# Performance work log

Measured on AMD Instinct MI355X. Metric: run time of the kernel, lower is better.

The kernel has to match this reference:

```python
import jax, jax.numpy as jnp
import numpy as np

LAG_SEQ = [1, 2, 3, 4, 5, 6, 7, 14, 21, 28]
MAX_LAG = 28
N_LAGS = 10
HID = 64
B, L, C = 256, 412, 3
CTX, HOR, NS = 336, 48, 100
IN_DIM = 15  # target + 10 lags + emb + last feat + log-scale + (C-2) mid feats


def lstm_cell(x, h, c, W_ih, W_hh, b_ih, b_hh):
    g = x @ W_ih.T + b_ih + h @ W_hh.T + b_hh
    i, f, gg, o = jnp.split(g, 4, axis=-1)
    c = jax.nn.sigmoid(f) * c + jax.nn.sigmoid(i) * jnp.tanh(gg)
    h = jax.nn.sigmoid(o) * jnp.tanh(c)
    return h, c


def lstm_layer(x, h, c, W_ih, W_hh, b_ih, b_hh):
    # x: [B, T, I] -> out [B, T, HID]; PyTorch gate order i,f,g,o
    xp = x @ W_ih.T + b_ih
    def step(carry, xt):
        h, c = carry
        g = xt + h @ W_hh.T + b_hh
        i, f, gg, o = jnp.split(g, 4, axis=-1)
        c = jax.nn.sigmoid(f) * c + jax.nn.sigmoid(i) * jnp.tanh(gg)
        h = jax.nn.sigmoid(o) * jnp.tanh(c)
        return (h, c), h
    (h, c), ys = jax.lax.scan(step, (h, c), jnp.swapaxes(xp, 0, 1))
    return jnp.swapaxes(ys, 0, 1), h, c


def head(out, w_df, b_df, w_loc, b_loc, w_scale, b_scale):
    # GluonTS-style StudentT output head
    df = 2.0 + jax.nn.softplus(jnp.dot(out, w_df) + b_df)
    loc = jnp.dot(out, w_loc) + b_loc
    scale = jax.nn.softplus(jnp.dot(out, w_scale) + b_scale)
    return df, loc, scale


def student_t_noise(key, df):
    kz, kg = jax.random.split(key)
    z = jax.random.normal(kz, df.shape, dtype=df.dtype)
    g = jax.random.gamma(kg, df * 0.5)  # chi2(df) = 2 * gamma(df/2)
    return z * jnp.sqrt(df / (2.0 * g))


def deepar_forward(X, pad_mask, W_ih0, W_hh0, b_ih0, b_hh0, W_ih1, W_hh1, b_ih1, b_hh1,
                   w_df, b_df, w_loc, b_loc, w_scale, b_scale, emb, H, context_length, n_samples):
    lag_idx = jnp.array(LAG_SEQ)
    Bd, Ld, Cd = X.shape
    ctx = context_length
    # zero out future targets, reversed observed target
    X = X.at[:, -H:, 0].set(0.0)
    past_target = jnp.flip(X[:, :-H, 0], axis=1)              # [B, L-H], newest first
    X = X[:, MAX_LAG:, :]
    pad_mask = pad_mask[:, MAX_LAG:]
    T = Ld - MAX_LAG
    # masked mean-abs scaling over the context window
    m = pad_mask[:, :ctx, None].astype(X.dtype)
    tscale = jnp.sum(jnp.abs(X[:, :ctx, :1]) * m, axis=1, keepdims=True) / jnp.maximum(
        jnp.sum(m, axis=1, keepdims=True), 1.0)
    tscale = jnp.maximum(tscale, 1e-10)                       # [B,1,1]
    Xs = X.at[:, :, 0].set(X[:, :, 0] / tscale[:, :, 0])
    past_target = past_target / tscale[:, :, 0]
    # context lags: step t gathers past_target[:, lag_seq + t], then flip over t
    idx = lag_idx[None, :] + jnp.arange(ctx)[:, None]         # [ctx, N_LAGS]
    ctx_lags = jnp.flip(past_target[:, idx], axis=1)          # [B, ctx, N_LAGS]
    lags = jnp.zeros((Bd, T, N_LAGS), X.dtype).at[:, :ctx].set(ctx_lags)
    emb_feat = jnp.broadcast_to(emb[0, 0], (Bd, T, 1))
    log_scale = jnp.broadcast_to(jnp.log(tscale[:, :, :1]), (Bd, T, 1))
    Xc = jnp.concatenate([Xs[:, :, :1], lags, emb_feat, Xs[:, :, -1:], log_scale,
                          Xs[:, :, 1:-1]], axis=2)            # [B, T, IN_DIM]
    inp = Xc[:, :-1, :]
    # context encoding with 2-layer LSTM
    z = jnp.zeros((Bd, HID), X.dtype)
    out0, h0, c0 = lstm_layer(inp[:, :ctx], z, z, W_ih0, W_hh0, b_ih0, b_hh0)
    out1, h1, c1 = lstm_layer(out0, z, z, W_ih1, W_hh1, b_ih1, b_hh1)
    df, loc, sc = head(out1, w_df, b_df, w_loc, b_loc, w_scale, b_scale)  # [B, ctx]
    # repeat_interleave over samples
    rep = lambda a: jnp.repeat(a, n_samples, axis=0)
    df, loc, sc = rep(df), rep(loc), rep(sc)
    tscale_flat = rep(tscale[:, 0, 0])                        # [NSB]
    key = jax.random.key(42)
    k_ctx, k_loop = jax.random.split(key)
    y_ctx = (loc + sc * student_t_noise(k_ctx, df)) * tscale_flat[:, None]  # [NSB, ctx]
    rows = jnp.swapaxes(rep(inp[:, ctx:ctx + H - 1, :]), 0, 1)  # [H-1, NSB, IN_DIM]
    buf0 = rep(past_target[:, :MAX_LAG])                       # [NSB, MAX_LAG]
    h0r, c0r, h1r, c1r = rep(h0), rep(c0), rep(h1), rep(c1)
    keys = jax.random.split(k_loop, H - 1)

    def step(carry, xt):
        prev, buf, h0, c0, h1, c1 = carry
        row, k = xt
        new_scaled = prev / tscale_flat
        buf2 = jnp.concatenate([new_scaled[:, None], buf], axis=1)  # [NSB, MAX_LAG+1]
        lag_f = buf2[:, lag_idx]                                    # [NSB, N_LAGS]
        row = row.at[:, 0].set(new_scaled)
        row = jax.lax.dynamic_update_slice(row, lag_f, (0, 1))
        row = jax.lax.stop_gradient(row)  # mirrors .clone().detach() in torch loop
        h0n, c0n = lstm_cell(row, h0, c0, W_ih0, W_hh0, b_ih0, b_hh0)
        h1n, c1n = lstm_cell(h0n, h1, c1, W_ih1, W_hh1, b_ih1, b_hh1)
        d, l, s = head(h1n, w_df, b_df, w_loc, b_loc, w_scale, b_scale)  # [NSB]
        y = (l + s * student_t_noise(k, d)) * tscale_flat
        return (y, buf2[:, :MAX_LAG], h0n, c0n, h1n, c1n), y

    init = (y_ctx[:, -1], buf0, h0r, c0r, h1r, c1r)
    _, ys = jax.lax.scan(step, init, (rows, keys))
    y_hat = jnp.concatenate([y_ctx, jnp.swapaxes(ys, 0, 1)], axis=1)  # [NSB, T-1]
    y_hat = y_hat.reshape(Bd, n_samples, T - 1)
    # torch.median returns the lower middle element for even n
    med = jnp.sort(y_hat, axis=1)[:, (n_samples - 1) // 2, :]
    return med[:, :, None]                                    # [B, T-1, 1]


def setup_inputs():
    key = jax.random.key(0)
    ks = jax.random.split(key, 20)
    rn = lambda k, shape, s=0.08: jax.random.normal(k, shape, dtype=jnp.float32) * s
    return {
        "X": jax.random.normal(ks[0], (B, L, C), dtype=jnp.float32),
        "pad_mask": jnp.ones((B, L), dtype=bool),
        "W_ih0": rn(ks[1], (4 * HID, IN_DIM)), "W_hh0": rn(ks[2], (4 * HID, HID)),
        "b_ih0": rn(ks[3], (4 * HID,)), "b_hh0": rn(ks[4], (4 * HID,)),
        "W_ih1": rn(ks[5], (4 * HID, HID)), "W_hh1": rn(ks[6], (4 * HID, HID)),
        "b_ih1": rn(ks[7], (4 * HID,)), "b_hh1": rn(ks[8], (4 * HID,)),
        "w_df": rn(ks[9], (HID,)), "b_df": rn(ks[10], ()),
        "w_loc": rn(ks[11], (HID,)), "b_loc": rn(ks[12], ()),
        "w_scale": rn(ks[13], (HID,)), "b_scale": rn(ks[14], ()),
        "emb": rn(ks[15], (1, 1)),
        "H": HOR, "context_length": CTX, "n_samples": NS,
    }


def reference(X, pad_mask, W_ih0, W_hh0, b_ih0, b_hh0, W_ih1, W_hh1, b_ih1, b_hh1,
              w_df, b_df, w_loc, b_loc, w_scale, b_scale, emb, H, context_length, n_samples):
    return deepar_forward(X, pad_mask, W_ih0, W_hh0, b_ih0, b_hh0, W_ih1, W_hh1, b_ih1, b_hh1,
                          w_df, b_df, w_loc, b_loc, w_scale, b_scale, emb,
                          H, context_length, n_samples)
```

## Files before the change

kernel.cpp:

```cpp
#include <hip/hip_runtime.h>
#include <stdint.h>
#include <stddef.h>

typedef uint32_t u32;
typedef float v2f __attribute__((ext_vector_type(2)));
typedef _Float16 f16;
typedef f16 half8 __attribute__((ext_vector_type(8)));
typedef float floatx4 __attribute__((ext_vector_type(4)));

#define NB    256
#define LFULL 412
#define NCH   3
#define CTX   336
#define NSAMP 100
#define TM1   383
#define HID   64
#define NIN   15
#define RTOT  25600
#define NCTXS 8601600u
#define NSTEP 47

#define DROWS   128
#define RPW     16
#define DBLOCKS (RTOT / DROWS)

#define HSTR    72

#define JAX_PARTITIONABLE 1

__device__ const int c_LAGS[10] = {1,2,3,4,5,6,7,14,21,28};

__device__ inline v2f bc2(float x) { v2f r; r[0] = x; r[1] = x; return r; }

__host__ __device__ inline void tf2x32(u32 k0, u32 k1, u32 x0, u32 x1, u32& o0, u32& o1) {
  const u32 ks2 = k0 ^ k1 ^ 0x1BD11BDAu;
#define TFR(r) { x0 += x1; x1 = (x1 << (r)) | (x1 >> (32 - (r))); x1 ^= x0; }
  x0 += k0; x1 += k1;
  TFR(13) TFR(15) TFR(26) TFR(6)
  x0 += k1; x1 += ks2 + 1u;
  TFR(17) TFR(29) TFR(16) TFR(24)
  x0 += ks2; x1 += k0 + 2u;
  TFR(13) TFR(15) TFR(26) TFR(6)
  x0 += k0; x1 += k1 + 3u;
  TFR(17) TFR(29) TFR(16) TFR(24)
  x0 += k1; x1 += ks2 + 4u;
  TFR(13) TFR(15) TFR(26) TFR(6)
  x0 += ks2; x1 += k0 + 5u;
#undef TFR
  o0 = x0; o1 = x1;
}

__host__ __device__ inline u32 split_word_legacy(u32 k0, u32 k1, u32 n, u32 j) {
  u32 o0, o1;
  if (j < n) { tf2x32(k0, k1, j, n + j, o0, o1); return o0; }
  tf2x32(k0, k1, j - n, j, o0, o1); return o1;
}

__host__ __device__ inline void jx_subkey(u32 k0, u32 k1, u32 n, u32 i, u32& s0, u32& s1) {
#if JAX_PARTITIONABLE
  (void)n; tf2x32(k0, k1, 0u, i, s0, s1);
#else
  s0 = split_word_legacy(k0, k1, n, 2u * i);
  s1 = split_word_legacy(k0, k1, n, 2u * i + 1u);
#endif
}
// ... 72 lines not shown
    u32 nk0, nk1, xk0, xk1, uk0, uk1;
    jx_subkey(K0, K1, 3u, 0u, nk0, nk1);
    jx_subkey(K0, K1, 3u, 1u, xk0, xk1);
    jx_subkey(K0, K1, 3u, 2u, uk0, uk1);
    K0 = nk0; K1 = nk1;
    float x, v;
    u32 c0 = xk0, c1 = xk1;
    do {
      u32 t0, t1, s0, s1;
      jx_subkey(c0, c1, 2u, 0u, t0, t1);
      jx_subkey(c0, c1, 2u, 1u, s0, s1);
      c0 = t0; c1 = t1;
      x = normal_from_bits(jx_bits(s0, s1, 1u, 0u));
      v = 1.0f + x * c;
    } while (v <= 0.0f);
    X = x * x;
    V = (v * v) * v;
    U = u01_from_bits(jx_bits(uk0, uk1, 1u, 0u));
  }
  const float sample = d * V;
  const float boost = boost_mask ? 1.0f : powf(u_boost, 1.0f / alpha_orig);
  return sample * boost;
}

__device__ inline float sigm(float x) {
  return __builtin_amdgcn_rcpf(1.0f + exp2f(-1.44269504f * x));
}
__device__ inline float tanh_fast(float x) {
  const float e = exp2f(2.88539008f * x);
  return 1.0f - 2.0f * __builtin_amdgcn_rcpf(e + 1.0f);
}
__device__ inline float softplusf(float x) { return fmaxf(x, 0.0f) + log1pf(expf(-fabsf(x))); }

__device__ inline float rl_f(float v, int l) {
  return __int_as_float(__builtin_amdgcn_readlane(__float_as_int(v), l));
}

enum : size_t {
  OFF_INP  = 0,
  OFF_CT   = OFF_INP + (size_t)NB * TM1 * NIN,
  OFF_TS   = OFF_CT + (size_t)NB * CTX,
  OFF_LTS  = OFF_TS + NB,
  OFF_DF   = OFF_LTS + NB,
  OFF_LOC  = OFF_DF + (size_t)NB * CTX,
  OFF_SC   = OFF_LOC + (size_t)NB * CTX,
  OFF_H0F  = OFF_SC + (size_t)NB * CTX,
  OFF_C0F  = OFF_H0F + (size_t)NB * HID,
  OFF_H1F  = OFF_C0F + (size_t)NB * HID,
  OFF_C1F  = OFF_H1F + (size_t)NB * HID,
  OFF_YH   = OFF_C1F + (size_t)NB * HID,
  OFF_WTX  = OFF_YH + (size_t)RTOT * TM1,
  OFF_WT00 = OFF_WTX + 4096,
  OFF_WT10 = OFF_WT00 + 16384,
  OFF_WT11 = OFF_WT10 + 16384,
  OFF_WH   = OFF_WT11 + 16384,
  OFF_RND  = OFF_WH + 27136,
  WS_FLOATS = OFF_RND + (size_t)NSTEP * RTOT * 4
};

#define WH_X   0
#define WH_00  4096
#define WH_10  20480
#define WH_11  36864
#define WH_HD  53248
#define WH_TOT 54272

__global__ void __launch_bounds__(256) wtrans_kernel(
    const float* __restrict__ Wih0, const float* __restrict__ Whh0,
    const float* __restrict__ Wih1, const float* __restrict__ Whh1,
    float* __restrict__ WTx, float* __restrict__ WT00,
    float* __restrict__ WT10, float* __restrict__ WT11)
{
  const int i = blockIdx.x * 256 + threadIdx.x;
  if (i < 4096) {
    const int k = i >> 8, g = i & 255;
    WTx[i] = (k < 15) ? Wih0[g * 15 + k] : 0.0f;
  } else if (i < 4096 + 16384) {
    const int j = i - 4096, k = j >> 8, g = j & 255;
    WT00[j] = Whh0[g * 64 + k];
  } else if (i < 4096 + 32768) {
    const int j = i - 4096 - 16384, k = j >> 8, g = j & 255;
    WT10[j] = Wih1[g * 64 + k];
  } else {
    const int j = i - 4096 - 32768, k = j >> 8, g = j & 255;
    WT11[j] = Whh1[g * 64 + k];
  }
}

__global__ void __launch_bounds__(256) wh_kernel(
    const float* __restrict__ Wih0, const float* __restrict__ Whh0,
    const float* __restrict__ Wih1, const float* __restrict__ Whh1,
    const float* __restrict__ bih0, const float* __restrict__ bhh0,
    const float* __restrict__ wdf, const float* __restrict__ wloc,
    const float* __restrict__ wsc,
    f16* __restrict__ WH)
{
  const int j = blockIdx.x * 256 + threadIdx.x;
  if (j < WH_00) {
    const int nt = j >> 8, rem = j & 255;
    const int l = rem >> 3, e = rem & 7;
    const int g = nt * 16 + (l & 15);
    const int k = (l >> 4) * 8 + e;
    WH[j] = (f16)((k < 15) ? Wih0[g * 15 + k] : (bih0[g] + bhh0[g]));
  } else if (j < WH_HD) {
    const float* W; int q;
    if (j < WH_10)      { W = Whh0; q = j - WH_00; }
    else if (j < WH_11) { W = Wih1; q = j - WH_10; }
    else                { W = Whh1; q = j - WH_11; }
    const int blk = q >> 9, rem = q & 511;
    const int l = rem >> 3, e = rem & 7;
    const int nt = blk >> 1, kc = blk & 1;
    const int g = nt * 16 + (l & 15);
    const int k = kc * 32 + (l >> 4) * 8 + e;
    WH[j] = (f16)W[g * 64 + k];
  } else {
    const int q = j - WH_HD;
    const int kc = q >> 9, rem = q & 511;
    const int l = rem >> 3, e = rem & 7;
    const int n = l & 15;
    const int k = kc * 32 + (l >> 4) * 8 + e;
// ... 10 lines not shown
{
  const int i = blockIdx.x * 256 + threadIdx.x;
  const int s = i / RTOT, rg = i - s * RTOT;
  u32 ks0, ks1, skz0, skz1, skg0, skg1;
  tf2x32(kl0, kl1, 0u, (u32)s, ks0, ks1);
  tf2x32(ks0, ks1, 0u, 0u, skz0, skz1);
  tf2x32(ks0, ks1, 0u, 1u, skg0, skg1);
  const float z = normal_from_bits(jx_bits(skz0, skz1, RTOT, (u32)rg));
  u32 gk0, gk1;
  jx_subkey(skg0, skg1, RTOT, (u32)rg, gk0, gk1);
  u32 K0, K1, S0, S1;
  jx_subkey(gk0, gk1, 2u, 0u, K0, K1);
  jx_subkey(gk0, gk1, 2u, 1u, S0, S1);
  u32 nk0, nk1, xk0, xk1, uk0, uk1;
  jx_subkey(K0, K1, 3u, 0u, nk0, nk1);
  jx_subkey(K0, K1, 3u, 1u, xk0, xk1);
  jx_subkey(K0, K1, 3u, 2u, uk0, uk1);
  u32 c0 = xk0, c1 = xk1, t0, t1, s0, s1;
  jx_subkey(c0, c1, 2u, 0u, t0, t1);
  jx_subkey(c0, c1, 2u, 1u, s0, s1);
  const float x1 = normal_from_bits(jx_bits(s0, s1, 1u, 0u));
  c0 = t0; c1 = t1;
  jx_subkey(c0, c1, 2u, 0u, t0, t1);
  jx_subkey(c0, c1, 2u, 1u, s0, s1);
  const float x2 = normal_from_bits(jx_bits(s0, s1, 1u, 0u));
  const float U1 = u01_from_bits(jx_bits(uk0, uk1, 1u, 0u));
  float* R = RND + (size_t)i * 4;
  R[0] = z; R[1] = x1; R[2] = x2; R[3] = U1;
}

__global__ void __launch_bounds__(256) prep_kernel(
    const float* __restrict__ X, const float* __restrict__ emb,
    float* __restrict__ inp, float* __restrict__ ct,
    float* __restrict__ tscale, float* __restrict__ ltscale)
{
  const int b = blockIdx.x, t = threadIdx.x;
  __shared__ float red[256];
  __shared__ float ts_sh;
  const float* Xb = X + (size_t)b * LFULL * NCH;
  float p = fabsf(Xb[(28 + t) * NCH]);
  if (t < 80) p += fabsf(Xb[(28 + 256 + t) * NCH]);
  red[t] = p;
  for (int st = 128; st > 0; st >>= 1) { __syncthreads(); if (t < st) red[t] += red[t + st]; }
  __syncthreads();
  if (t == 0) {
    float ts = red[0] / 336.0f;
    ts = fmaxf(ts, 1e-10f);
    tscale[b] = ts; ltscale[b] = logf(ts); ts_sh = ts;
  }
  __syncthreads();
  const float ts = ts_sh;
  const float lts = logf(ts);
  const float ev = emb[0];
  for (int idx = t; idx < TM1 * NIN; idx += 256) {
    const int tt = idx / NIN, f = idx - tt * NIN;
    float val;
    if (f == 0)       val = (tt < CTX) ? Xb[(28 + tt) * NCH] / ts : 0.0f;
    else if (f <= 10) val = (tt < CTX) ? Xb[(28 + tt - c_LAGS[f - 1]) * NCH] / ts : 0.0f;
    else if (f == 11) val = ev;
    else if (f == 12) val = Xb[(28 + tt) * NCH + 2];
    else if (f == 13) val = lts;
    else              val = Xb[(28 + tt) * NCH + 1];
    inp[(size_t)(b * TM1 + tt) * NIN + f] = val;
    if (f == 0 && tt < CTX) ct[b * CTX + tt] = val;
  }
}

__global__ void __launch_bounds__(256) ctx_lstm_kernel(
    const float* __restrict__ inp,
    const float* __restrict__ WTx, const float* __restrict__ WT00,
    const float* __restrict__ WT10, const float* __restrict__ WT11,
    const float* __restrict__ bih0, const float* __restrict__ bhh0,
    const float* __restrict__ bih1, const float* __restrict__ bhh1,
    const float* __restrict__ wdf, const float* __restrict__ bdfp,
    const float* __restrict__ wloc, const float* __restrict__ blocp,
    const float* __restrict__ wsc, const float* __restrict__ bscp,
    float* __restrict__ dfo, float* __restrict__ loco, float* __restrict__ sco,
    float* __restrict__ h0f, float* __restrict__ c0f,
    float* __restrict__ h1f, float* __restrict__ c1f)
{
  const int b = blockIdx.x, t = threadIdx.x;
  const int lane = t & 63, w = t >> 6;
  const int gbase = lane << 2;
  __shared__ __align__(16) float gA[4][256];
  __shared__ __align__(16) float gB[4][256];

  const float bs0 = bih0[lane]       + bhh0[lane];
  const float bs1 = bih0[64 + lane]  + bhh0[64 + lane];
  const float bs2 = bih0[128 + lane] + bhh0[128 + lane];
  const float bs3 = bih0[192 + lane] + bhh0[192 + lane];
  const float bs4 = bih1[lane]       + bhh1[lane];
  const float bs5 = bih1[64 + lane]  + bhh1[64 + lane];
  const float bs6 = bih1[128 + lane] + bhh1[128 + lane];
  const float bs7 = bih1[192 + lane] + bhh1[192 + lane];
  const float wdfv = wdf[lane], wlocv = wloc[lane], wscv = wsc[lane];
  const float bdf = bdfp[0], bloc = blocp[0], bsc = bscp[0];

  float h0r = 0.f, h1r = 0.f, c0r = 0.f, c1r = 0.f;
  const float* inb = inp + (size_t)b * TM1 * NIN;
  const int kx = w * 4;
  const int kh = w * 16;

  for (int tt = 0; tt < CTX; tt++) {
    float xr = 0.f;
    if (lane < 15) xr = inb[tt * NIN + lane];

    v2f aA = bc2(0.0f), aB = bc2(0.0f);
#pragma unroll
    for (int kk = 0; kk < 4; kk++) {
      const int k = kx + kk;
      const float4 wv = *(const float4*)&WTx[(k << 8) + gbase];
      v2f wlo, whi; wlo[0] = wv.x; wlo[1] = wv.y; whi[0] = wv.z; whi[1] = wv.w;
      const v2f hk = bc2(rl_f(xr, k));
      aA += wlo * hk; aB += whi * hk;
    }
#pragma unroll
    for (int kk = 0; kk < 16; kk++) {
      const int k = kh + kk;
      const float4 wv = *(const float4*)&WT00[(k << 8) + gbase];
      v2f wlo, whi; wlo[0] = wv.x; wlo[1] = wv.y; whi[0] = wv.z; whi[1] = wv.w;
      const v2f hk = bc2(rl_f(h0r, k));
      aA += wlo * hk; aB += whi * hk;
    }
    {
      float4 gv; gv.x = aA[0]; gv.y = aA[1]; gv.z = aB[0]; gv.w = aB[1];
      *(float4*)&gA[w][gbase] = gv;
    }
    __syncthreads();

    {
      float gi = ((gA[0][lane]       + gA[1][lane])       + gA[2][lane])       + gA[3][lane];
      float gf = ((gA[0][64 + lane]  + gA[1][64 + lane])  + gA[2][64 + lane])  + gA[3][64 + lane];
      float gg = ((gA[0][128 + lane] + gA[1][128 + lane]) + gA[2][128 + lane]) + gA[3][128 + lane];
      float go = ((gA[0][192 + lane] + gA[1][192 + lane]) + gA[2][192 + lane]) + gA[3][192 + lane];
      gi += bs0; gf += bs1; gg += bs2; go += bs3;
      c0r = sigm(gf) * c0r + sigm(gi) * tanh_fast(gg);
      h0r = sigm(go) * tanh_fast(c0r);
    }

    aA = bc2(0.0f); aB = bc2(0.0f);
#pragma unroll
    for (int kk = 0; kk < 16; kk++) {
      const int k = kh + kk;
      const float4 wv = *(const float4*)&WT10[(k << 8) + gbase];
      v2f wlo, whi; wlo[0] = wv.x; wlo[1] = wv.y; whi[0] = wv.z; whi[1] = wv.w;
      const v2f hk = bc2(rl_f(h0r, k));
      aA += wlo * hk; aB += whi * hk;
    }
#pragma unroll
    for (int kk = 0; kk < 16; kk++) {
      const int k = kh + kk;
      const float4 wv = *(const float4*)&WT11[(k << 8) + gbase];
      v2f wlo, whi; wlo[0] = wv.x; wlo[1] = wv.y; whi[0] = wv.z; whi[1] = wv.w;
      const v2f hk = bc2(rl_f(h1r, k));
      aA += wlo * hk; aB += whi * hk;
    }
    {
      float4 gv; gv.x = aA[0]; gv.y = aA[1]; gv.z = aB[0]; gv.w = aB[1];
      *(float4*)&gB[w][gbase] = gv;
    }
    __syncthreads();

    {
      float gi = ((gB[0][lane]       + gB[1][lane])       + gB[2][lane])       + gB[3][lane];
      float gf = ((gB[0][64 + lane]  + gB[1][64 + lane])  + gB[2][64 + lane])  + gB[3][64 + lane];
      float gg = ((gB[0][128 + lane] + gB[1][128 + lane]) + gB[2][128 + lane]) + gB[3][128 + lane];
      float go = ((gB[0][192 + lane] + gB[1][192 + lane]) + gB[2][192 + lane]) + gB[3][192 + lane];
      gi += bs4; gf += bs5; gg += bs6; go += bs7;
      c1r = sigm(gf) * c1r + sigm(gi) * tanh_fast(gg);
      h1r = sigm(go) * tanh_fast(c1r);
      if (w == 0) {
        float pd = h1r * wdfv, pl = h1r * wlocv, ps = h1r * wscv;
#pragma unroll
        for (int off = 32; off > 0; off >>= 1) {
          pd += __shfl_down(pd, off, 64);
          pl += __shfl_down(pl, off, 64);
          ps += __shfl_down(ps, off, 64);
        }
        if (lane == 0) {
          dfo[b * CTX + tt]  = 2.0f + softplusf(pd + bdf);
          loco[b * CTX + tt] = pl + bloc;
          sco[b * CTX + tt]  = softplusf(ps + bsc);
        }
      }
    }
  }
  if (w == 0) {
    h0f[b * 64 + lane] = h0r; c0f[b * 64 + lane] = c0r;
    h1f[b * 64 + lane] = h1r; c1f[b * 64 + lane] = c1r;
  }
}

__global__ void __launch_bounds__(256) ctx_sample_kernel(
    const float* __restrict__ df, const float* __restrict__ loc, const float* __restrict__ sc,
    const float* __restrict__ tscale, float* __restrict__ yhat,
    u32 kz0, u32 kz1, u32 kg0, u32 kg1)
{
  const int i = blockIdx.x * 256 + threadIdx.x;
  const int r = i / CTX, t = i - r * CTX;
  const int b = r / NSAMP;
  const float dfv = df[b * CTX + t], lv = loc[b * CTX + t], sv = sc[b * CTX + t];
  const float z = normal_from_bits(jx_bits(kz0, kz1, NCTXS, (u32)i));
  u32 gk0, gk1;
  jx_subkey(kg0, kg1, NCTXS, (u32)i, gk0, gk1);
  const float g = jax_gamma_one(gk0, gk1, dfv * 0.5f);
  const float y = (lv + sv * (z * sqrtf(dfv / (2.0f * g)))) * tscale[b];
  yhat[(size_t)r * TM1 + t] = y;
}

__global__ void __attribute__((amdgpu_flat_work_group_size(512, 512),
                               amdgpu_waves_per_eu(2, 2)))
dec_persist_kernel(
    const float* __restrict__ inp, const float* __restrict__ tscale,
    const f16* __restrict__ WH, const float* __restrict__ emb,
    const float* __restrict__ bih1, const float* __restrict__ bhh1,
    const float* __restrict__ bdfp, const float* __restrict__ blocp,
    const float* __restrict__ bscp,
    const float* __restrict__ h0f, const float* __restrict__ c0f,
    const float* __restrict__ h1f, const float* __restrict__ c1f,
    const float* __restrict__ ct, const float* __restrict__ RND,
    float* __restrict__ yhat, u32 kl0, u32 kl1)
{
  const int t    = threadIdx.x;
// ... 100 lines not shown
        if (sl <= 10) {
          xh[row][sl] = hist[row][(s - c_LAGS[sl - 1]) & 31];
        } else if (sl == 12) {
          xh[row][sl] = fst[rsel[row]][s][0];
        } else if (sl == 14) {
          xh[row][sl] = fst[rsel[row]][s][1];
        }
      }
    }

    const half8 ax  = *(const half8*)axp;
    const half8 a00 = *(const half8*)&h0h[arow * HSTR + kg * 8];
    const half8 a01 = *(const half8*)&h0h[arow * HSTR + 32 + kg * 8];
#pragma unroll
    for (int tq = 0; tq < 4; tq++) {
      floatx4 ai = {0.f, 0.f, 0.f, 0.f};
      floatx4 af = {0.f, 0.f, 0.f, 0.f};
      floatx4 ag = {0.f, 0.f, 0.f, 0.f};
      floatx4 ao = {0.f, 0.f, 0.f, 0.f};
      ai = __builtin_amdgcn_mfma_f32_16x16x32_f16(ax, BFR(WH_X + (tq)      * 256), ai, 0, 0, 0);
      af = __builtin_amdgcn_mfma_f32_16x16x32_f16(ax, BFR(WH_X + (4 + tq)  * 256), af, 0, 0, 0);
      ag = __builtin_amdgcn_mfma_f32_16x16x32_f16(ax, BFR(WH_X + (8 + tq)  * 256), ag, 0, 0, 0);
      ao = __builtin_amdgcn_mfma_f32_16x16x32_f16(ax, BFR(WH_X + (12 + tq) * 256), ao, 0, 0, 0);
      ai = __builtin_amdgcn_mfma_f32_16x16x32_f16(a00, BFR(WH_00 + ((tq) * 2 + 0)      * 512), ai, 0, 0, 0);
      ai = __builtin_amdgcn_mfma_f32_16x16x32_f16(a01, BFR(WH_00 + ((tq) * 2 + 1)      * 512), ai, 0, 0, 0);
      af = __builtin_amdgcn_mfma_f32_16x16x32_f16(a00, BFR(WH_00 + ((4 + tq) * 2 + 0)  * 512), af, 0, 0, 0);
      af = __builtin_amdgcn_mfma_f32_16x16x32_f16(a01, BFR(WH_00 + ((4 + tq) * 2 + 1)  * 512), af, 0, 0, 0);
      ag = __builtin_amdgcn_mfma_f32_16x16x32_f16(a00, BFR(WH_00 + ((8 + tq) * 2 + 0)  * 512), ag, 0, 0, 0);
      ag = __builtin_amdgcn_mfma_f32_16x16x32_f16(a01, BFR(WH_00 + ((8 + tq) * 2 + 1)  * 512), ag, 0, 0, 0);
      ao = __builtin_amdgcn_mfma_f32_16x16x32_f16(a00, BFR(WH_00 + ((12 + tq) * 2 + 0) * 512), ao, 0, 0, 0);
      ao = __builtin_amdgcn_mfma_f32_16x16x32_f16(a01, BFR(WH_00 + ((12 + tq) * 2 + 1) * 512), ao, 0, 0, 0);
#pragma unroll
      for (int rr = 0; rr < 4; rr++) {
        const float gi = ai[rr], gf = af[rr], gg = ag[rr], go = ao[rr];
        float cc = c0reg[rr][tq];
        cc = sigm(gf) * cc + sigm(gi) * tanh_fast(gg);
        c0reg[rr][tq] = cc;
        h0h[(r0 + kg * 4 + rr) * HSTR + tq * 16 + c16] = (f16)(sigm(go) * tanh_fast(cc));
      }
      __builtin_amdgcn_sched_barrier(0);
    }

    const half8 a10a = *(const half8*)&h0h[arow * HSTR + kg * 8];
    const half8 a10b = *(const half8*)&h0h[arow * HSTR + 32 + kg * 8];
    const half8 a11a = *(const half8*)&h1h[arow * HSTR + kg * 8];
    const half8 a11b = *(const half8*)&h1h[arow * HSTR + 32 + kg * 8];
#pragma unroll
    for (int tq = 0; tq < 4; tq++) {
      const float bi = b1L[0][tq][c16];
      const float bf = b1L[1][tq][c16];
      const float bg = b1L[2][tq][c16];
      const float bo = b1L[3][tq][c16];
      floatx4 ai = {bi, bi, bi, bi};
      floatx4 af = {bf, bf, bf, bf};
      floatx4 ag = {bg, bg, bg, bg};
      floatx4 ao = {bo, bo, bo, bo};
      ai = __builtin_amdgcn_mfma_f32_16x16x32_f16(a10a, BFR(WH_10 + ((tq) * 2 + 0)      * 512), ai, 0, 0, 0);
      ai = __builtin_amdgcn_mfma_f32_16x16x32_f16(a10b, BFR(WH_10 + ((tq) * 2 + 1)      * 512), ai, 0, 0, 0);
      ai = __builtin_amdgcn_mfma_f32_16x16x32_f16(a11a, BFR(WH_11 + ((tq) * 2 + 0)      * 512), ai, 0, 0, 0);
      ai = __builtin_amdgcn_mfma_f32_16x16x32_f16(a11b, BFR(WH_11 + ((tq) * 2 + 1)      * 512), ai, 0, 0, 0);
      af = __builtin_amdgcn_mfma_f32_16x16x32_f16(a10a, BFR(WH_10 + ((4 + tq) * 2 + 0)  * 512), af, 0, 0, 0);
      af = __builtin_amdgcn_mfma_f32_16x16x32_f16(a10b, BFR(WH_10 + ((4 + tq) * 2 + 1)  * 512), af, 0, 0, 0);
      af = __builtin_amdgcn_mfma_f32_16x16x32_f16(a11a, BFR(WH_11 + ((4 + tq) * 2 + 0)  * 512), af, 0, 0, 0);
      af = __builtin_amdgcn_mfma_f32_16x16x32_f16(a11b, BFR(WH_11 + ((4 + tq) * 2 + 1)  * 512), af, 0, 0, 0);
      ag = __builtin_amdgcn_mfma_f32_16x16x32_f16(a10a, BFR(WH_10 + ((8 + tq) * 2 + 0)  * 512), ag, 0, 0, 0);
      ag = __builtin_amdgcn_mfma_f32_16x16x32_f16(a10b, BFR(WH_10 + ((8 + tq) * 2 + 1)  * 512), ag, 0, 0, 0);
      ag = __builtin_amdgcn_mfma_f32_16x16x32_f16(a11a, BFR(WH_11 + ((8 + tq) * 2 + 0)  * 512), ag, 0, 0, 0);
      ag = __builtin_amdgcn_mfma_f32_16x16x32_f16(a11b, BFR(WH_11 + ((8 + tq) * 2 + 1)  * 512), ag, 0, 0, 0);
      ao = __builtin_amdgcn_mfma_f32_16x16x32_f16(a10a, BFR(WH_10 + ((12 + tq) * 2 + 0) * 512), ao, 0, 0, 0);
      ao = __builtin_amdgcn_mfma_f32_16x16x32_f16(a10b, BFR(WH_10 + ((12 + tq) * 2 + 1) * 512), ao, 0, 0, 0);
      ao = __builtin_amdgcn_mfma_f32_16x16x32_f16(a11a, BFR(WH_11 + ((12 + tq) * 2 + 0) * 512), ao, 0, 0, 0);
      ao = __builtin_amdgcn_mfma_f32_16x16x32_f16(a11b, BFR(WH_11 + ((12 + tq) * 2 + 1) * 512), ao, 0, 0, 0);
#pragma unroll
      for (int rr = 0; rr < 4; rr++) {
        const float gi = ai[rr], gf = af[rr], gg = ag[rr], go = ao[rr];
        float cc = c1reg[rr][tq];
        cc = sigm(gf) * cc + sigm(gi) * tanh_fast(gg);
        c1reg[rr][tq] = cc;
        h1h[(r0 + kg * 4 + rr) * HSTR + tq * 16 + c16] = (f16)(sigm(go) * tanh_fast(cc));
      }
      __builtin_amdgcn_sched_barrier(0);
    }

    {
      const half8 an0 = *(const half8*)&h1h[arow * HSTR + kg * 8];
      const half8 an1 = *(const half8*)&h1h[arow * HSTR + 32 + kg * 8];
      floatx4 hd = {0.f, 0.f, 0.f, 0.f};
      hd = __builtin_amdgcn_mfma_f32_16x16x32_f16(an0, BFR(WH_HD + 0 * 512), hd, 0, 0, 0);
      hd = __builtin_amdgcn_mfma_f32_16x16x32_f16(an1, BFR(WH_HD + 1 * 512), hd, 0, 0, 0);
      if (c16 == 0) {
#pragma unroll
        for (int rr = 0; rr < 4; rr++)
          dfL[r0 + kg * 4 + rr] = 2.0f + softplusf(hd[rr] + bdf);
      } else if (c16 == 1) {
#pragma unroll
        for (int rr = 0; rr < 4; rr++)
          locL[r0 + kg * 4 + rr] = hd[rr] + bloc;
      } else if (c16 == 2) {
#pragma unroll
        for (int rr = 0; rr < 4; rr++)
          scL[r0 + kg * 4 + rr] = softplusf(hd[rr] + bsc);
      }
    }

    if (lane < RPW) {
      const int row = r0 + lane, rg = base + row;
      const float4 R = *(const float4*)(RND + ((size_t)s * RTOT + rg) * 4);
      const float dfv = dfL[row], lv = locL[row], scv = scL[row];
      const float z = R.x;
      const float alpha = dfv * 0.5f;
      float gam;
      {
// ... 57 lines not shown
                              void* d_out, int out_size, void* d_ws, size_t ws_size,
                              hipStream_t stream) {
  (void)in_sizes; (void)n_in; (void)out_size; (void)ws_size;
  const float* X     = (const float*)d_in[0];
  const float* Wih0  = (const float*)d_in[2];
  const float* Whh0  = (const float*)d_in[3];
  const float* bih0  = (const float*)d_in[4];
  const float* bhh0  = (const float*)d_in[5];
  const float* Wih1  = (const float*)d_in[6];
  const float* Whh1  = (const float*)d_in[7];
  const float* bih1  = (const float*)d_in[8];
  const float* bhh1  = (const float*)d_in[9];
  const float* wdf   = (const float*)d_in[10];
  const float* bdf   = (const float*)d_in[11];
  const float* wloc  = (const float*)d_in[12];
  const float* bloc  = (const float*)d_in[13];
  const float* wsc   = (const float*)d_in[14];
  const float* bsc   = (const float*)d_in[15];
  const float* emb   = (const float*)d_in[16];

  float* wsf = (float*)d_ws;
  float* inp  = wsf + OFF_INP;
  float* ct   = wsf + OFF_CT;
  float* ts   = wsf + OFF_TS;
  float* lts  = wsf + OFF_LTS;
  float* dfp  = wsf + OFF_DF;
  float* locp = wsf + OFF_LOC;
  float* scp  = wsf + OFF_SC;
  float* h0f  = wsf + OFF_H0F;
  float* c0f  = wsf + OFF_C0F;
  float* h1f  = wsf + OFF_H1F;
  float* c1f  = wsf + OFF_C1F;
  float* yhat = wsf + OFF_YH;
  float* wtx  = wsf + OFF_WTX;
  float* wt00 = wsf + OFF_WT00;
  float* wt10 = wsf + OFF_WT10;
  float* wt11 = wsf + OFF_WT11;
  f16*   wh   = (f16*)(wsf + OFF_WH);
  float* rnd  = wsf + OFF_RND;

  const u32 key0 = 0u, key1 = 42u;
  u32 kc0, kc1, kl0, kl1;
  jx_subkey(key0, key1, 2u, 0u, kc0, kc1);
  jx_subkey(key0, key1, 2u, 1u, kl0, kl1);
  u32 kz0, kz1, kg0, kg1;
  jx_subkey(kc0, kc1, 2u, 0u, kz0, kz1);
  jx_subkey(kc0, kc1, 2u, 1u, kg0, kg1);

  wtrans_kernel<<<208, 256, 0, stream>>>(Wih0, Whh0, Wih1, Whh1, wtx, wt00, wt10, wt11);
  wh_kernel<<<212, 256, 0, stream>>>(Wih0, Whh0, Wih1, Whh1, bih0, bhh0,
                                     wdf, wloc, wsc, wh);
  rnd_dec_kernel<<<(NSTEP * RTOT) / 256, 256, 0, stream>>>(rnd, kl0, kl1);
  prep_kernel<<<NB, 256, 0, stream>>>(X, emb, inp, ct, ts, lts);
  ctx_lstm_kernel<<<NB, 256, 0, stream>>>(inp, wtx, wt00, wt10, wt11,
                                          bih0, bhh0, bih1, bhh1,
                                          wdf, bdf, wloc, bloc, wsc, bsc,
                                          dfp, locp, scp, h0f, c0f, h1f, c1f);
  ctx_sample_kernel<<<NCTXS / 256, 256, 0, stream>>>(dfp, locp, scp, ts, yhat, kz0, kz1, kg0, kg1);
  dec_persist_kernel<<<DBLOCKS, 512, 0, stream>>>(inp, ts, wh, emb,
                                                  bih1, bhh1,
                                                  bdf, bloc, bsc,
                                                  h0f, c0f, h1f, c1f, ct, rnd, yhat, kl0, kl1);
  median_kernel<<<(NB * TM1) / 4, 256, 0, stream>>>(yhat, (float*)d_out);
}
```

Measured before the change: 2.072 ms.

## Replace fp32 per-sequence context LSTM with batched fp16 MFMA kernel

The context-window LSTM, which ran one sequence per block with fp32 FMA, readlane broadcasts and shared-memory reductions, is replaced by a kernel that batches 16 sequences per block and computes all gate GEMMs with 16x16x32 fp16 MFMA, reusing the packed fp16 weight buffer from the decoder. The prep kernel now also writes an fp16 padded context input with a constant-one column so the layer-0 bias is folded into the weights, and the fp32 weight transpose kernel is removed. Only 16 blocks are launched, so most of the GPU sits idle during this stage. Keeping the hidden state and weights in fp16 for the context pass costs some precision.

```diff
diff --git a/kernel.cpp b/kernel.cpp
--- a/kernel.cpp
+++ b/kernel.cpp
@@ -3,7 +3,6 @@
 #include <stddef.h>
 
 typedef uint32_t u32;
-typedef float v2f __attribute__((ext_vector_type(2)));
 typedef _Float16 f16;
 typedef f16 half8 __attribute__((ext_vector_type(8)));
 typedef float floatx4 __attribute__((ext_vector_type(4)));
@@ -24,13 +23,12 @@
 #define RPW     16
 #define DBLOCKS (RTOT / DROWS)
 
+#define CROWS   16
 #define HSTR    72
 
 #define JAX_PARTITIONABLE 1
 
 __device__ const int c_LAGS[10] = {1,2,3,4,5,6,7,14,21,28};
-
-__device__ inline v2f bc2(float x) { v2f r; r[0] = x; r[1] = x; return r; }
 
 __host__ __device__ inline void tf2x32(u32 k0, u32 k1, u32 x0, u32 x1, u32& o0, u32& o1) {
   const u32 ks2 = k0 ^ k1 ^ 0x1BD11BDAu;
@@ -169,10 +167,6 @@
 }
 __device__ inline float softplusf(float x) { return fmaxf(x, 0.0f) + log1pf(expf(-fabsf(x))); }
 
-__device__ inline float rl_f(float v, int l) {
-  return __int_as_float(__builtin_amdgcn_readlane(__float_as_int(v), l));
-}
-
 enum : size_t {
   OFF_INP  = 0,
   OFF_CT   = OFF_INP + (size_t)NB * TM1 * NIN,
@@ -186,12 +180,9 @@
   OFF_H1F  = OFF_C0F + (size_t)NB * HID,
   OFF_C1F  = OFF_H1F + (size_t)NB * HID,
   OFF_YH   = OFF_C1F + (size_t)NB * HID,
-  OFF_WTX  = OFF_YH + (size_t)RTOT * TM1,
-  OFF_WT00 = OFF_WTX + 4096,
-  OFF_WT10 = OFF_WT00 + 16384,
-  OFF_WT11 = OFF_WT10 + 16384,
-  OFF_WH   = OFF_WT11 + 16384,
-  OFF_RND  = OFF_WH + 27136,
+  OFF_WH   = OFF_YH + (size_t)RTOT * TM1,
+  OFF_XC   = OFF_WH + 27136,
+  OFF_RND  = OFF_XC + ((size_t)NB * CTX * 16) / 2,
   WS_FLOATS = OFF_RND + (size_t)NSTEP * RTOT * 4
 };
 
@@ -201,28 +192,6 @@
 #define WH_11  36864
 #define WH_HD  53248
 #define WH_TOT 54272
-
-__global__ void __launch_bounds__(256) wtrans_kernel(
-    const float* __restrict__ Wih0, const float* __restrict__ Whh0,
-    const float* __restrict__ Wih1, const float* __restrict__ Whh1,
-    float* __restrict__ WTx, float* __restrict__ WT00,
-    float* __restrict__ WT10, float* __restrict__ WT11)
-{
-  const int i = blockIdx.x * 256 + threadIdx.x;
-  if (i < 4096) {
-    const int k = i >> 8, g = i & 255;
-    WTx[i] = (k < 15) ? Wih0[g * 15 + k] : 0.0f;
-  } else if (i < 4096 + 16384) {
-    const int j = i - 4096, k = j >> 8, g = j & 255;
-    WT00[j] = Whh0[g * 64 + k];
-  } else if (i < 4096 + 32768) {
-    const int j = i - 4096 - 16384, k = j >> 8, g = j & 255;
-    WT10[j] = Wih1[g * 64 + k];
-  } else {
-    const int j = i - 4096 - 32768, k = j >> 8, g = j & 255;
-    WT11[j] = Whh1[g * 64 + k];
-  }
-}
 
 __global__ void __launch_bounds__(256) wh_kernel(
     const float* __restrict__ Wih0, const float* __restrict__ Whh0,
@@ -299,6 +268,7 @@
 __global__ void __launch_bounds__(256) prep_kernel(
     const float* __restrict__ X, const float* __restrict__ emb,
     float* __restrict__ inp, float* __restrict__ ct,
+    f16* __restrict__ xc,
     float* __restrict__ tscale, float* __restrict__ ltscale)
 {
   const int b = blockIdx.x, t = threadIdx.x;
@@ -329,133 +299,172 @@
     else if (f == 13) val = lts;
     else              val = Xb[(28 + tt) * NCH + 1];
     inp[(size_t)(b * TM1 + tt) * NIN + f] = val;
-    if (f == 0 && tt < CTX) ct[b * CTX + tt] = val;
-  }
-}
-
-__global__ void __launch_bounds__(256) ctx_lstm_kernel(
-    const float* __restrict__ inp,
-    const float* __restrict__ WTx, const float* __restrict__ WT00,
-    const float* __restrict__ WT10, const float* __restrict__ WT11,
-    const float* __restrict__ bih0, const float* __restrict__ bhh0,
+    if (tt < CTX) {
+      xc[((size_t)(b * CTX + tt)) * 16 + f] = (f16)val;
+      if (f == 0) {
+        ct[b * CTX + tt] = val;
+        xc[((size_t)(b * CTX + tt)) * 16 + 15] = (f16)1.0f;
+      }
+    }
+  }
+}
+
+__global__ void __launch_bounds__(256) ctx_mfma_kernel(
+    const f16* __restrict__ XC, const f16* __restrict__ WH,
     const float* __restrict__ bih1, const float* __restrict__ bhh1,
-    const float* __restrict__ wdf, const float* __restrict__ bdfp,
-    const float* __restrict__ wloc, const float* __restrict__ blocp,
-    const float* __restrict__ wsc, const float* __restrict__ bscp,
+    const float* __restrict__ bdfp, const float* __restrict__ blocp,
+    const float* __restrict__ bscp,
     float* __restrict__ dfo, float* __restrict__ loco, float* __restrict__ sco,
     float* __restrict__ h0f, float* __restrict__ c0f,
     float* __restrict__ h1f, float* __restrict__ c1f)
 {
-  const int b = blockIdx.x, t = threadIdx.x;
-  const int lane = t & 63, w = t >> 6;
-  const int gbase = lane << 2;
-  __shared__ __align__(16) float gA[4][256];
-  __shared__ __align__(16) float gB[4][256];
-
-  const float bs0 = bih0[lane]       + bhh0[lane];
-  const float bs1 = bih0[64 + lane]  + bhh0[64 + lane];
-  const float bs2 = bih0[128 + lane] + bhh0[128 + lane];
-  const float bs3 = bih0[192 + lane] + bhh0[192 + lane];
-  const float bs4 = bih1[lane]       + bhh1[lane];
-  const float bs5 = bih1[64 + lane]  + bhh1[64 + lane];
-  const float bs6 = bih1[128 + lane] + bhh1[128 + lane];
-  const float bs7 = bih1[192 + lane] + bhh1[192 + lane];
-  const float wdfv = wdf[lane], wlocv = wloc[lane], wscv = wsc[lane];
+  const int t    = threadIdx.x;
+  const int lane = t & 63;
+  const int w    = t >> 6;
+  const int c16  = lane & 15;
+  const int kg   = lane >> 4;
+  const int base = blockIdx.x * CROWS;
+
+  __shared__ __align__(16) f16 wgt[WH_TOT];
+  __shared__ __align__(16) f16 h0h[CROWS * HSTR];
+  __shared__ __align__(16) f16 h1h[CROWS * HSTR];
+  __shared__ __align__(16) f16 xzero[32];
+
+  for (int i = w; i < WH_TOT / 512; i += 4) {
+    const int off = i * 512;
+    __builtin_amdgcn_global_load_lds(
+        (const __attribute__((address_space(1))) void*)(WH + off + lane * 8),
+        (__attribute__((address_space(3))) void*)(wgt + off), 16, 0, 0);
+  }
+  for (int idx = t; idx < CROWS * HSTR; idx += 256) { h0h[idx] = (f16)0.0f; h1h[idx] = (f16)0.0f; }
+  if (t < 32) xzero[t] = (f16)0.0f;
+
+  float b1r[4];
+#pragma unroll
+  for (int gq = 0; gq < 4; gq++) {
+    const int g = gq * 64 + w * 16 + c16;
+    b1r[gq] = bih1[g] + bhh1[g];
+  }
   const float bdf = bdfp[0], bloc = blocp[0], bsc = bscp[0];
 
-  float h0r = 0.f, h1r = 0.f, c0r = 0.f, c1r = 0.f;
-  const float* inb = inp + (size_t)b * TM1 * NIN;
-  const int kx = w * 4;
-  const int kh = w * 16;
+  float c0reg[4] = {0.f, 0.f, 0.f, 0.f};
+  float c1reg[4] = {0.f, 0.f, 0.f, 0.f};
+
+  const int arow = c16;
+  const f16* axbase = XC + (size_t)(base + c16) * CTX * 16;
+
+  __syncthreads();
+
+  half8 ax = (kg < 2) ? *(const half8*)(axbase + 0 * 16 + kg * 8)
+                      : *(const half8*)&xzero[0];
+
+#define BFR(off) (*(const half8*)&wgt[(off) + lane * 8])
 
   for (int tt = 0; tt < CTX; tt++) {
-    float xr = 0.f;
-    if (lane < 15) xr = inb[tt * NIN + lane];
-
-    v2f aA = bc2(0.0f), aB = bc2(0.0f);
-#pragma unroll
-    for (int kk = 0; kk < 4; kk++) {
-      const int k = kx + kk;
-      const float4 wv = *(const float4*)&WTx[(k << 8) + gbase];
-      v2f wlo, whi; wlo[0] = wv.x; wlo[1] = wv.y; whi[0] = wv.z; whi[1] = wv.w;
-      const v2f hk = bc2(rl_f(xr, k));
-      aA += wlo * hk; aB += whi * hk;
-    }
-#pragma unroll
-    for (int kk = 0; kk < 16; kk++) {
-      const int k = kh + kk;
-      const float4 wv = *(const float4*)&WT00[(k << 8) + gbase];
-      v2f wlo, whi; wlo[0] = wv.x; wlo[1] = wv.y; whi[0] = wv.z; whi[1] = wv.w;
-      const v2f hk = bc2(rl_f(h0r, k));
-      aA += wlo * hk; aB += whi * hk;
-    }
+    const half8 axc  = ax;
+    const half8 a00  = *(const half8*)&h0h[arow * HSTR + kg * 8];
+    const half8 a01  = *(const half8*)&h0h[arow * HSTR + 32 + kg * 8];
+    const half8 a11a = *(const half8*)&h1h[arow * HSTR + kg * 8];
+    const half8 a11b = *(const half8*)&h1h[arow * HSTR + 32 + kg * 8];
+    __syncthreads();
+
+    if (tt + 1 < CTX && kg < 2)
+      ax = *(const half8*)(axbase + (tt + 1) * 16 + kg * 8);
+
     {
-      float4 gv; gv.x = aA[0]; gv.y = aA[1]; gv.z = aB[0]; gv.w = aB[1];
-      *(float4*)&gA[w][gbase] = gv;
+      floatx4 ai = {0.f, 0.f, 0.f, 0.f};
+      floatx4 af = {0.f, 0.f, 0.f, 0.f};
+      floatx4 ag = {0.f, 0.f, 0.f, 0.f};
+      floatx4 ao = {0.f, 0.f, 0.f, 0.f};
+      ai = __builtin_amdgcn_mfma_f32_16x16x32_f16(axc, BFR(WH_X + (w)      * 256), ai, 0, 0, 0);
+      af = __builtin_amdgcn_mfma_f32_16x16x32_f16(axc, BFR(WH_X + (4 + w)  * 256), af, 0, 0, 0);
+      ag = __builtin_amdgcn_mfma_f32_16x16x32_f16(axc, BFR(WH_X + (8 + w)  * 256), ag, 0, 0, 0);
+      ao = __builtin_amdgcn_mfma_f32_16x16x32_f16(axc, BFR(WH_X + (12 + w) * 256), ao, 0, 0, 0);
+      ai = __builtin_amdgcn_mfma_f32_16x16x32_f16(a00, BFR(WH_00 + ((w) * 2 + 0)      * 512), ai, 0, 0, 0);
+      ai = __builtin_amdgcn_mfma_f32_16x16x32_f16(a01, BFR(WH_00 + ((w) * 2 + 1)      * 512), ai, 0, 0, 0);
+      af = __builtin_amdgcn_mfma_f32_16x16x32_f16(a00, BFR(WH_00 + ((4 + w) * 2 + 0)  * 512), af, 0, 0, 0);
+      af = __builtin_amdgcn_mfma_f32_16x16x32_f16(a01, BFR(WH_00 + ((4 + w) * 2 + 1)  * 512), af, 0, 0, 0);
+      ag = __builtin_amdgcn_mfma_f32_16x16x32_f16(a00, BFR(WH_00 + ((8 + w) * 2 + 0)  * 512), ag, 0, 0, 0);
+      ag = __builtin_amdgcn_mfma_f32_16x16x32_f16(a01, BFR(WH_00 + ((8 + w) * 2 + 1)  * 512), ag, 0, 0, 0);
+      ao = __builtin_amdgcn_mfma_f32_16x16x32_f16(a00, BFR(WH_00 + ((12 + w) * 2 + 0) * 512), ao, 0, 0, 0);
+      ao = __builtin_amdgcn_mfma_f32_16x16x32_f16(a01, BFR(WH_00 + ((12 + w) * 2 + 1) * 512), ao, 0, 0, 0);
+#pragma unroll
+      for (int rr = 0; rr < 4; rr++) {
+        float cc = c0reg[rr];
+        cc = sigm(af[rr]) * cc + sigm(ai[rr]) * tanh_fast(ag[rr]);
+        c0reg[rr] = cc;
+        h0h[(kg * 4 + rr) * HSTR + w * 16 + c16] = (f16)(sigm(ao[rr]) * tanh_fast(cc));
+      }
     }
     __syncthreads();
 
     {
-      float gi = ((gA[0][lane]       + gA[1][lane])       + gA[2][lane])       + gA[3][lane];
-      float gf = ((gA[0][64 + lane]  + gA[1][64 + lane])  + gA[2][64 + lane])  + gA[3][64 + lane];
-      float gg = ((gA[0][128 + lane] + gA[1][128 + lane]) + gA[2][128 + lane]) + gA[3][128 + lane];
-      float go = ((gA[0][192 + lane] + gA[1][192 + lane]) + gA[2][192 + lane]) + gA[3][192 + lane];
-      gi += bs0; gf += bs1; gg += bs2; go += bs3;
-      c0r = sigm(gf) * c0r + sigm(gi) * tanh_fast(gg);
-      h0r = sigm(go) * tanh_fast(c0r);
-    }
-
-    aA = bc2(0.0f); aB = bc2(0.0f);
-#pragma unroll
-    for (int kk = 0; kk < 16; kk++) {
-      const int k = kh + kk;
-      const float4 wv = *(const float4*)&WT10[(k << 8) + gbase];
-      v2f wlo, whi; wlo[0] = wv.x; wlo[1] = wv.y; whi[0] = wv.z; whi[1] = wv.w;
-      const v2f hk = bc2(rl_f(h0r, k));
-      aA += wlo * hk; aB += whi * hk;
-    }
-#pragma unroll
-    for (int kk = 0; kk < 16; kk++) {
-      const int k = kh + kk;
-      const float4 wv = *(const float4*)&WT11[(k << 8) + gbase];
-      v2f wlo, whi; wlo[0] = wv.x; wlo[1] = wv.y; whi[0] = wv.z; whi[1] = wv.w;
-      const v2f hk = bc2(rl_f(h1r, k));
-      aA += wlo * hk; aB += whi * hk;
-    }
-    {
-      float4 gv; gv.x = aA[0]; gv.y = aA[1]; gv.z = aB[0]; gv.w = aB[1];
-      *(float4*)&gB[w][gbase] = gv;
+      const half8 a10a = *(const half8*)&h0h[arow * HSTR + kg * 8];
+      const half8 a10b = *(const half8*)&h0h[arow * HSTR + 32 + kg * 8];
+      floatx4 ai = {b1r[0], b1r[0], b1r[0], b1r[0]};
+      floatx4 af = {b1r[1], b1r[1], b1r[1], b1r[1]};
+      floatx4 ag = {b1r[2], b1r[2], b1r[2], b1r[2]};
+      floatx4 ao = {b1r[3], b1r[3], b1r[3], b1r[3]};
+      ai = __builtin_amdgcn_mfma_f32_16x16x32_f16(a10a, BFR(WH_10 + ((w) * 2 + 0)      * 512), ai, 0, 0, 0);
+      ai = __builtin_amdgcn_mfma_f32_16x16x32_f16(a10b, BFR(WH_10 + ((w) * 2 + 1)      * 512), ai, 0, 0, 0);
+      ai = __builtin_amdgcn_mfma_f32_16x16x32_f16(a11a, BFR(WH_11 + ((w) * 2 + 0)      * 512), ai, 0, 0, 0);
+      ai = __builtin_amdgcn_mfma_f32_16x16x32_f16(a11b, BFR(WH_11 + ((w) * 2 + 1)      * 512), ai, 0, 0, 0);
+      af = __builtin_amdgcn_mfma_f32_16x16x32_f16(a10a, BFR(WH_10 + ((4 + w) * 2 + 0)  * 512), af, 0, 0, 0);
+      af = __builtin_amdgcn_mfma_f32_16x16x32_f16(a10b, BFR(WH_10 + ((4 + w) * 2 + 1)  * 512), af, 0, 0, 0);
+      af = __builtin_amdgcn_mfma_f32_16x16x32_f16(a11a, BFR(WH_11 + ((4 + w) * 2 + 0)  * 512), af, 0, 0, 0);
+      af = __builtin_amdgcn_mfma_f32_16x16x32_f16(a11b, BFR(WH_11 + ((4 + w) * 2 + 1)  * 512), af, 0, 0, 0);
+      ag = __builtin_amdgcn_mfma_f32_16x16x32_f16(a10a, BFR(WH_10 + ((8 + w) * 2 + 0)  * 512), ag, 0, 0, 0);
+      ag = __builtin_amdgcn_mfma_f32_16x16x32_f16(a10b, BFR(WH_10 + ((8 + w) * 2 + 1)  * 512), ag, 0, 0, 0);
+      ag = __builtin_amdgcn_mfma_f32_16x16x32_f16(a11a, BFR(WH_11 + ((8 + w) * 2 + 0)  * 512), ag, 0, 0, 0);
+      ag = __builtin_amdgcn_mfma_f32_16x16x32_f16(a11b, BFR(WH_11 + ((8 + w) * 2 + 1)  * 512), ag, 0, 0, 0);
+      ao = __builtin_amdgcn_mfma_f32_16x16x32_f16(a10a, BFR(WH_10 + ((12 + w) * 2 + 0) * 512), ao, 0, 0, 0);
+      ao = __builtin_amdgcn_mfma_f32_16x16x32_f16(a10b, BFR(WH_10 + ((12 + w) * 2 + 1) * 512), ao, 0, 0, 0);
+      ao = __builtin_amdgcn_mfma_f32_16x16x32_f16(a11a, BFR(WH_11 + ((12 + w) * 2 + 0) * 512), ao, 0, 0, 0);
+      ao = __builtin_amdgcn_mfma_f32_16x16x32_f16(a11b, BFR(WH_11 + ((12 + w) * 2 + 1) * 512), ao, 0, 0, 0);
+#pragma unroll
+      for (int rr = 0; rr < 4; rr++) {
+        float cc = c1reg[rr];
+        cc = sigm(af[rr]) * cc + sigm(ai[rr]) * tanh_fast(ag[rr]);
+        c1reg[rr] = cc;
+        h1h[(kg * 4 + rr) * HSTR + w * 16 + c16] = (f16)(sigm(ao[rr]) * tanh_fast(cc));
+      }
     }
     __syncthreads();
 
-    {
-      float gi = ((gB[0][lane]       + gB[1][lane])       + gB[2][lane])       + gB[3][lane];
-      float gf = ((gB[0][64 + lane]  + gB[1][64 + lane])  + gB[2][64 + lane])  + gB[3][64 + lane];
-      float gg = ((gB[0][128 + lane] + gB[1][128 + lane]) + gB[2][128 + lane]) + gB[3][128 + lane];
-      float go = ((gB[0][192 + lane] + gB[1][192 + lane]) + gB[2][192 + lane]) + gB[3][192 + lane];
-      gi += bs4; gf += bs5; gg += bs6; go += bs7;
-      c1r = sigm(gf) * c1r + sigm(gi) * tanh_fast(gg);
-      h1r = sigm(go) * tanh_fast(c1r);
-      if (w == 0) {
-        float pd = h1r * wdfv, pl = h1r * wlocv, ps = h1r * wscv;
-#pragma unroll
-        for (int off = 32; off > 0; off >>= 1) {
-          pd += __shfl_down(pd, off, 64);
-          pl += __shfl_down(pl, off, 64);
-          ps += __shfl_down(ps, off, 64);
-        }
-        if (lane == 0) {
-          dfo[b * CTX + tt]  = 2.0f + softplusf(pd + bdf);
-          loco[b * CTX + tt] = pl + bloc;
-          sco[b * CTX + tt]  = softplusf(ps + bsc);
-        }
+    if (w == 0) {
+      const half8 an0 = *(const half8*)&h1h[arow * HSTR + kg * 8];
+      const half8 an1 = *(const half8*)&h1h[arow * HSTR + 32 + kg * 8];
+      floatx4 hd = {0.f, 0.f, 0.f, 0.f};
+      hd = __builtin_amdgcn_mfma_f32_16x16x32_f16(an0, BFR(WH_HD + 0 * 512), hd, 0, 0, 0);
+      hd = __builtin_amdgcn_mfma_f32_16x16x32_f16(an1, BFR(WH_HD + 1 * 512), hd, 0, 0, 0);
+      if (c16 == 0) {
+#pragma unroll
+        for (int rr = 0; rr < 4; rr++)
+          dfo[(base + kg * 4 + rr) * CTX + tt] = 2.0f + softplusf(hd[rr] + bdf);
+      } else if (c16 == 1) {
+#pragma unroll
+        for (int rr = 0; rr < 4; rr++)
+          loco[(base + kg * 4 + rr) * CTX + tt] = hd[rr] + bloc;
+      } else if (c16 == 2) {
+#pragma unroll
+        for (int rr = 0; rr < 4; rr++)
+          sco[(base + kg * 4 + rr) * CTX + tt] = softplusf(hd[rr] + bsc);
       }
     }
   }
-  if (w == 0) {
-    h0f[b * 64 + lane] = h0r; c0f[b * 64 + lane] = c0r;
-    h1f[b * 64 + lane] = h1r; c1f[b * 64 + lane] = c1r;
-  }
+
+#pragma unroll
+  for (int rr = 0; rr < 4; rr++) {
+    const int b = base + kg * 4 + rr;
+    c0f[b * 64 + w * 16 + c16] = c0reg[rr];
+    c1f[b * 64 + w * 16 + c16] = c1reg[rr];
+  }
+  for (int idx = t; idx < CROWS * 64; idx += 256) {
+    const int row = idx >> 6, hid = idx & 63;
+    h0f[(base + row) * 64 + hid] = (float)h0h[row * HSTR + hid];
+    h1f[(base + row) * 64 + hid] = (float)h1h[row * HSTR + hid];
+  }
+#undef BFR
 }
 
 __global__ void __launch_bounds__(256) ctx_sample_kernel(
@@ -622,11 +631,10 @@
       ao = __builtin_amdgcn_mfma_f32_16x16x32_f16(a01, BFR(WH_00 + ((12 + tq) * 2 + 1) * 512), ao, 0, 0, 0);
 #pragma unroll
       for (int rr = 0; rr < 4; rr++) {
-        const float gi = ai[rr], gf = af[rr], gg = ag[rr], go = ao[rr];
         float cc = c0reg[rr][tq];
-        cc = sigm(gf) * cc + sigm(gi) * tanh_fast(gg);
+        cc = sigm(af[rr]) * cc + sigm(ai[rr]) * tanh_fast(ag[rr]);
         c0reg[rr][tq] = cc;
-        h0h[(r0 + kg * 4 + rr) * HSTR + tq * 16 + c16] = (f16)(sigm(go) * tanh_fast(cc));
+        h0h[(r0 + kg * 4 + rr) * HSTR + tq * 16 + c16] = (f16)(sigm(ao[rr]) * tanh_fast(cc));
       }
       __builtin_amdgcn_sched_barrier(0);
     }
@@ -663,11 +671,10 @@
       ao = __builtin_amdgcn_mfma_f32_16x16x32_f16(a11b, BFR(WH_11 + ((12 + tq) * 2 + 1) * 512), ao, 0, 0, 0);
 #pragma unroll
       for (int rr = 0; rr < 4; rr++) {
-        const float gi = ai[rr], gf = af[rr], gg = ag[rr], go = ao[rr];
         float cc = c1reg[rr][tq];
-        cc = sigm(gf) * cc + sigm(gi) * tanh_fast(gg);
+        cc = sigm(af[rr]) * cc + sigm(ai[rr]) * tanh_fast(ag[rr]);
         c1reg[rr][tq] = cc;
-        h1h[(r0 + kg * 4 + rr) * HSTR + tq * 16 + c16] = (f16)(sigm(go) * tanh_fast(cc));
+        h1h[(r0 + kg * 4 + rr) * HSTR + tq * 16 + c16] = (f16)(sigm(ao[rr]) * tanh_fast(cc));
       }
       __builtin_amdgcn_sched_barrier(0);
     }
@@ -791,11 +798,8 @@
   float* h1f  = wsf + OFF_H1F;
   float* c1f  = wsf + OFF_C1F;
   float* yhat = wsf + OFF_YH;
-  float* wtx  = wsf + OFF_WTX;
-  float* wt00 = wsf + OFF_WT00;
-  float* wt10 = wsf + OFF_WT10;
-  float* wt11 = wsf + OFF_WT11;
   f16*   wh   = (f16*)(wsf + OFF_WH);
+  f16*   xc   = (f16*)(wsf + OFF_XC);
   float* rnd  = wsf + OFF_RND;
 
   const u32 key0 = 0u, key1 = 42u;
@@ -806,15 +810,14 @@
   jx_subkey(kc0, kc1, 2u, 0u, kz0, kz1);
   jx_subkey(kc0, kc1, 2u, 1u, kg0, kg1);
 
-  wtrans_kernel<<<208, 256, 0, stream>>>(Wih0, Whh0, Wih1, Whh1, wtx, wt00, wt10, wt11);
   wh_kernel<<<212, 256, 0, stream>>>(Wih0, Whh0, Wih1, Whh1, bih0, bhh0,
                                      wdf, wloc, wsc, wh);
   rnd_dec_kernel<<<(NSTEP * RTOT) / 256, 256, 0, stream>>>(rnd, kl0, kl1);
-  prep_kernel<<<NB, 256, 0, stream>>>(X, emb, inp, ct, ts, lts);
-  ctx_lstm_kernel<<<NB, 256, 0, stream>>>(inp, wtx, wt00, wt10, wt11,
-                                          bih0, bhh0, bih1, bhh1,
-                                          wdf, bdf, wloc, bloc, wsc, bsc,
-                                          dfp, locp, scp, h0f, c0f, h1f, c1f);
+  prep_kernel<<<NB, 256, 0, stream>>>(X, emb, inp, ct, xc, ts, lts);
+  ctx_mfma_kernel<<<NB / CROWS, 256, 0, stream>>>(xc, wh,
+                                                  bih1, bhh1, bdf, bloc, bsc,
+                                                  dfp, locp, scp,
+                                                  h0f, c0f, h1f, c1f);
   ctx_sample_kernel<<<NCTXS / 256, 256, 0, stream>>>(dfp, locp, scp, ts, yhat, kz0, kz1, kg0, kg1);
   dec_persist_kernel<<<DBLOCKS, 512, 0, stream>>>(inp, ts, wh, emb,
                                                   bih1, bhh1,
```

Result: slower. 2.944 ms (+42.1%).
